# Kernel optimization log

Measured on AMD Instinct MI355X. Metric: run time of the kernel, lower is better.

## Reference

```python
import jax, jax.numpy as jnp
import numpy as np

NUM_HEAD = 16

def setup_inputs() -> dict:
    rk = jax.random.key(0)
    k1, k2, k3, k4, k5 = jax.random.split(rk, 5)
    B, Sq, Skv, D = 4, 2048, 2048, 1024
    return {
        "query": jax.random.normal(k1, (B, Sq, D), dtype=jnp.float32),
        "key":   jax.random.normal(k2, (B, Skv, D), dtype=jnp.float32),
        "value": jax.random.normal(k3, (B, Skv, D), dtype=jnp.float32),
        "W": jax.random.normal(k4, (D, D), dtype=jnp.float32) * (D ** -0.5),
        "b": jax.random.normal(k5, (D,), dtype=jnp.float32) * 0.01,
    }

def reference(query, key, value, W, b):
    B, Sq, D = query.shape
    H = NUM_HEAD
    hd = D // H
    # chunk(num_head, -1) == split last dim into H contiguous heads
    q = query.reshape(B, Sq, H, hd)
    k = key.reshape(B, -1, H, hd)
    v = value.reshape(B, -1, H, hd)
    # scores[b,h,q,k] = (Q_h K_h^T) / sqrt(embedding_dim)  (full dim, per source)
    scores = jnp.einsum('bqhd,bkhd->bhqk', q, k) / jnp.sqrt(jnp.float32(D))
    # nn.Softmax(dim=1) on a [B, q, kv] matrix -> softmax over the QUERY axis
    attn = jax.nn.softmax(scores, axis=2)
    out = jnp.einsum('bhqk,bkhd->bqhd', attn, v).reshape(B, Sq, D)
    # final linear: x @ W^T + b
    return out @ W.T + b
```

## Files before the change

### kernel.cpp

```cpp
#include <hip/hip_runtime.h>

#define NH    16
#define HD    64
#define SQ    2048
#define SKV   2048
#define DM    1024

typedef __attribute__((ext_vector_type(8))) __bf16 bf16x8;
typedef __attribute__((ext_vector_type(4))) __bf16 bf16x4;
typedef __attribute__((ext_vector_type(4))) float  f32x4;

#define ASYNC16(gp, lp)                                                        \
    __builtin_amdgcn_global_load_lds(                                          \
        (const __attribute__((address_space(1))) void*)(gp),                   \
        (__attribute__((address_space(3))) void*)(lp), 16, 0, 0)

#if __has_builtin(__builtin_amdgcn_exp2f)
#define EXPS(x) __builtin_amdgcn_exp2f((x) * 0.04508422f)
#else
#define EXPS(x) __expf((x) * 0.03125f)
#endif

static __device__ __forceinline__ int swz(int row, int chunk) {
    return (row << 6) + (((chunk) ^ (row & 7)) << 3);
}

static __device__ __forceinline__ bf16x4 cvt4(float4 v) {
    bf16x4 r;
    r[0] = (__bf16)v.x; r[1] = (__bf16)v.y; r[2] = (__bf16)v.z; r[3] = (__bf16)v.w;
    return r;
}

__global__ void kprep_all(const float* __restrict__ q, const float* __restrict__ k,
                          const float* __restrict__ W,
                          __bf16* __restrict__ Qh, __bf16* __restrict__ Kh,
                          __bf16* __restrict__ Wb) {
    int bid = blockIdx.x;
    if (bid < 8192) {
        const float* src = (bid < 4096) ? q : k;
        __bf16* dst = (bid < 4096) ? Qh : Kh;
        size_t g = (size_t)(bid & 4095) * 256 + threadIdx.x;
        size_t o = g * 8;
        int c  = (int)(o & 63);
        int s  = (int)((o >> 6) & 2047);
        int bh = (int)(o >> 17);
        int b = bh >> 4, h = bh & 15;
        const float* p = src + ((size_t)(b * SQ + s)) * DM + h * HD + c;
        float4 v0 = *(const float4*)p;
        float4 v1 = *(const float4*)(p + 4);
        bf16x8 r;
        r[0] = (__bf16)v0.x; r[1] = (__bf16)v0.y; r[2] = (__bf16)v0.z; r[3] = (__bf16)v0.w;
        r[4] = (__bf16)v1.x; r[5] = (__bf16)v1.y; r[6] = (__bf16)v1.z; r[7] = (__bf16)v1.w;
        *(bf16x8*)(dst + o) = r;
    } else {
        int i = (bid - 8192) * 256 + threadIdx.x;
        float4 v = *(const float4*)(W + (size_t)i * 4);
        *(bf16x4*)(Wb + (size_t)i * 4) = cvt4(v);
    }
}

__global__ __launch_bounds__(512, 4) void kz(const __bf16* __restrict__ Qh,
                                             const __bf16* __restrict__ Kh,
                                             const __bf16* __restrict__ v,
                                             __bf16* __restrict__ Vt);

__global__ __launch_bounds__(512, 4) void kz(const __bf16* __restrict__ Qh,
                                             const __bf16* __restrict__ Kh,
                                             const __bf16* __restrict__ vv,
                                             __bf16* __restrict__ Vt) {
    const float* v = (const float*)vv;
    const int bh = blockIdx.x;
    const int kb = blockIdx.y;
    const int b = bh >> 4, h = bh & 15;
    const int t = threadIdx.x;
    const int w = t >> 6, lane = t & 63;
    const int lo16 = lane & 15, quad = lane >> 4;
    const int wub = (t & 448) << 3;

    __shared__ __bf16 Ks[256 * 64];
    __shared__ __bf16 Qs[2][64 * 64];
    __shared__ float  Zs[256];

    const __bf16* kbase = Kh + ((size_t)bh * SKV + kb * 256) * HD;
    const __bf16* qbase = Qh + (size_t)bh * SQ * HD;

#pragma unroll
    for (int i = 0; i < 4; ++i) {
        int ci = i * 512 + t;
        int row = ci >> 3;
        int c = (ci & 7) ^ (row & 7);
        ASYNC16(kbase + row * 64 + c * 8, &Ks[i * 4096 + wub]);
    }
    {
        int ci = t;
        int row = ci >> 3;
        int c = (ci & 7) ^ (row & 7);
        ASYNC16(qbase + row * 64 + c * 8, &Qs[0][wub]);
    }
    __syncthreads();

    bf16x8 bk[2][2];
#pragma unroll
    for (int nt = 0; nt < 2; ++nt)
#pragma unroll
        for (int dh = 0; dh < 2; ++dh)
            bk[nt][dh] = *(const bf16x8*)(&Ks[swz(w * 32 + nt * 16 + lo16, dh * 4 + quad)]);

    float zacc[2] = {0.f, 0.f};

    for (int qt = 0; qt < 32; ++qt) {
        const int cur = qt & 1, nxt = cur ^ 1;
        if (qt < 31) {
            int ci = t;
            int row = ci >> 3;
            int c = (ci & 7) ^ (row & 7);
            ASYNC16(qbase + (size_t)(qt + 1) * 64 * HD + row * 64 + c * 8,
                    &Qs[nxt][wub]);
        }

        __builtin_amdgcn_s_setprio(1);
#pragma unroll
        for (int mt = 0; mt < 4; ++mt) {
            bf16x8 aq0 = *(const bf16x8*)(&Qs[cur][swz(mt * 16 + lo16, quad)]);
            bf16x8 aq1 = *(const bf16x8*)(&Qs[cur][swz(mt * 16 + lo16, 4 + quad)]);
#pragma unroll
            for (int nt = 0; nt < 2; ++nt) {
                f32x4 acc = {0.f, 0.f, 0.f, 0.f};
                acc = __builtin_amdgcn_mfma_f32_16x16x32_bf16(aq0, bk[nt][0], acc, 0, 0, 0);
                acc = __builtin_amdgcn_mfma_f32_16x16x32_bf16(aq1, bk[nt][1], acc, 0, 0, 0);
                zacc[nt] += EXPS(acc[0]) + EXPS(acc[1]) + EXPS(acc[2]) + EXPS(acc[3]);
            }
        }
        __builtin_amdgcn_s_setprio(0);
        __syncthreads();
    }

#pragma unroll
    for (int nt = 0; nt < 2; ++nt) {
        float s = zacc[nt];
        s += __shfl_xor(s, 16, 64);
        s += __shfl_xor(s, 32, 64);
        if (lane < 16) Zs[w * 32 + nt * 16 + lane] = s;
    }
    __syncthreads();

    {
        int kcol = t & 255, dh2 = t >> 8;
        float rz = 1.0f / Zs[kcol];
        const float* vrow = v + ((size_t)(b * SKV) + kb * 256 + kcol) * DM + h * HD + dh2 * 32;
        size_t vtb = (size_t)bh * HD * SKV + kb * 256 + kcol;
#pragma unroll
        for (int dc = 0; dc < 2; ++dc) {
            float4 a0 = *(const float4*)(vrow + dc * 16 + 0);
            float4 a1 = *(const float4*)(vrow + dc * 16 + 4);
            float4 a2 = *(const float4*)(vrow + dc * 16 + 8);
            float4 a3 = *(const float4*)(vrow + dc * 16 + 12);
            float tmp[16] = {a0.x, a0.y, a0.z, a0.w, a1.x, a1.y, a1.z, a1.w,
                             a2.x, a2.y, a2.z, a2.w, a3.x, a3.y, a3.z, a3.w};
#pragma unroll
            for (int j = 0; j < 16; ++j)
                Vt[vtb + (size_t)(dh2 * 32 + dc * 16 + j) * SKV] = (__bf16)(tmp[j] * rz);
        }
    }
}

__global__ __launch_bounds__(512, 4) void kattn(const __bf16* __restrict__ Qh,
                                                const __bf16* __restrict__ Kh,
                                                const __bf16* __restrict__ Vt,
                                                __bf16* __restrict__ O) {
    const int bh = blockIdx.x;
    const int qb = blockIdx.y;
    const int b = bh >> 4, h = bh & 15;
    const int t = threadIdx.x;
    const int w = t >> 6, lane = t & 63;
    const int lo16 = lane & 15, quad = lane >> 4;
    const int wub = (t & 448) << 3;

    __shared__ __bf16 Ks[2][64 * 64];
    __shared__ __bf16 Vts[2][64 * 64];
    __shared__ __bf16 Es[8][32 * 64];

    const __bf16* qgb = Qh + ((size_t)bh * SQ + qb * 256 + w * 32) * HD;
    const __bf16* kgbase = Kh + (size_t)bh * SKV * HD;
    const __bf16* vtgbase = Vt + (size_t)bh * HD * SKV;

    {
        int ci = t;
        int row = ci >> 3;
        int c = (ci & 7) ^ (row & 7);
        ASYNC16(kgbase + row * 64 + c * 8, &Ks[0][wub]);
        ASYNC16(vtgbase + (size_t)row * SKV + c * 8, &Vts[0][wub]);
    }

    bf16x8 qf[2][2];
#pragma unroll
    for (int qt = 0; qt < 2; ++qt)
#pragma unroll
        for (int dh = 0; dh < 2; ++dh)
            qf[qt][dh] = *(const bf16x8*)(qgb + (size_t)(qt * 16 + lo16) * HD
                                          + (dh * 4 + quad) * 8);

    f32x4 oacc[2][4];
    f32x4 zero = {0.f, 0.f, 0.f, 0.f};
#pragma unroll
    for (int qt = 0; qt < 2; ++qt)
#pragma unroll
        for (int nt = 0; nt < 4; ++nt)
            oacc[qt][nt] = zero;

    __syncthreads();

    __bf16* Ew = &Es[w][0];

    for (int kt = 0; kt < 32; ++kt) {
        const int cur = kt & 1, nxt = cur ^ 1;
        if (kt < 31) {
            int ci = t;
            int row = ci >> 3;
            int c = (ci & 7) ^ (row & 7);
            ASYNC16(kgbase + (size_t)(kt + 1) * 64 * HD + row * 64 + c * 8,
                    &Ks[nxt][wub]);
            ASYNC16(vtgbase + (size_t)row * SKV + (kt + 1) * 64 + c * 8,
                    &Vts[nxt][wub]);
        }

        __builtin_amdgcn_s_setprio(1);
#pragma unroll
        for (int ktile = 0; ktile < 4; ++ktile) {
            bf16x8 ak0 = *(const bf16x8*)(&Ks[cur][swz(ktile * 16 + lo16, quad)]);
            bf16x8 ak1 = *(const bf16x8*)(&Ks[cur][swz(ktile * 16 + lo16, 4 + quad)]);
#pragma unroll
            for (int qt = 0; qt < 2; ++qt) {
                f32x4 s = zero;
                s = __builtin_amdgcn_mfma_f32_16x16x32_bf16(ak0, qf[qt][0], s, 0, 0, 0);
                s = __builtin_amdgcn_mfma_f32_16x16x32_bf16(ak1, qf[qt][1], s, 0, 0, 0);
                bf16x4 e;
                e[0] = (__bf16)EXPS(s[0]);
                e[1] = (__bf16)EXPS(s[1]);
                e[2] = (__bf16)EXPS(s[2]);
                e[3] = (__bf16)EXPS(s[3]);
                int er = qt * 16 + lo16;
                *(bf16x4*)(&Ew[(er << 6) + ((((2 * ktile + (quad >> 1))) ^ (er & 7)) << 3)
                               + (quad & 1) * 4]) = e;
            }
        }

#pragma unroll
        for (int kk2 = 0; kk2 < 2; ++kk2) {
            bf16x8 ae[2];
#pragma unroll
            for (int qt = 0; qt < 2; ++qt)
                ae[qt] = *(const bf16x8*)(&Ew[swz(qt * 16 + lo16, kk2 * 4 + quad)]);
#pragma unroll
            for (int nt = 0; nt < 4; ++nt) {
                bf16x8 bv = *(const bf16x8*)(&Vts[cur][swz(nt * 16 + lo16, kk2 * 4 + quad)]);
#pragma unroll
                for (int qt = 0; qt < 2; ++qt)
                    oacc[qt][nt] = __builtin_amdgcn_mfma_f32_16x16x32_bf16(ae[qt], bv, oacc[qt][nt], 0, 0, 0);
            }
        }
        __builtin_amdgcn_s_setprio(0);
        __syncthreads();
    }

    size_t obase = ((size_t)(b * SQ) + qb * 256 + w * 32) * DM + h * HD;
#pragma unroll
    for (int qt = 0; qt < 2; ++qt)
#pragma unroll
        for (int nt = 0; nt < 4; ++nt)
#pragma unroll
            for (int r = 0; r < 4; ++r)
                O[obase + (size_t)(qt * 16 + quad * 4 + r) * DM + nt * 16 + lo16] =
                    (__bf16)oacc[qt][nt][r];
}

__global__ __launch_bounds__(256, 2) void kproj(const __bf16* __restrict__ A,
                                                const __bf16* __restrict__ Wb,
                                                const float* __restrict__ bias,
                                                float* __restrict__ out) {
    const int nb = blockIdx.x;
    const int mb = blockIdx.y;
    const int t = threadIdx.x;
    const int w = t >> 6, lane = t & 63;
    const int lo16 = lane & 15, quad = lane >> 4;
    const int wm = w & 1, wn = w >> 1;
    const int wub = (t & 192) << 3;

    __shared__ __bf16 As[2][128 * 64];
    __shared__ __bf16 Bs[2][128 * 64];

    f32x4 acc[4][4];
    f32x4 zero = {0.f, 0.f, 0.f, 0.f};
#pragma unroll
    for (int mt = 0; mt < 4; ++mt)
#pragma unroll
        for (int nt = 0; nt < 4; ++nt)
            acc[mt][nt] = zero;

    const __bf16* abase = A + (size_t)(mb * 128) * DM;
    const __bf16* wbase = Wb + (size_t)(nb * 128) * DM;

#pragma unroll
    for (int i = 0; i < 4; ++i) {
        int ci = i * 256 + t;
        int row = ci >> 3;
        int c = (ci & 7) ^ (row & 7);
        ASYNC16(abase + (size_t)row * DM + c * 8, &As[0][i * 2048 + wub]);
        ASYNC16(wbase + (size_t)row * DM + c * 8, &Bs[0][i * 2048 + wub]);
    }
    __syncthreads();

    for (int kt = 0; kt < 16; ++kt) {
        const int cur = kt & 1, nxt = cur ^ 1;
        if (kt < 15) {
#pragma unroll
            for (int i = 0; i < 4; ++i) {
                int ci = i * 256 + t;
                int row = ci >> 3;
                int c = (ci & 7) ^ (row & 7);
                ASYNC16(abase + (size_t)row * DM + (kt + 1) * 64 + c * 8, &As[nxt][i * 2048 + wub]);
                ASYNC16(wbase + (size_t)row * DM + (kt + 1) * 64 + c * 8, &Bs[nxt][i * 2048 + wub]);
            }
        }

#pragma unroll
        for (int ks = 0; ks < 2; ++ks) {
            bf16x8 av[4], bv[4];
#pragma unroll
            for (int mt = 0; mt < 4; ++mt)
                av[mt] = *(const bf16x8*)(&As[cur][swz(wm * 64 + mt * 16 + lo16, ks * 4 + quad)]);
#pragma unroll
            for (int nt = 0; nt < 4; ++nt)
                bv[nt] = *(const bf16x8*)(&Bs[cur][swz(wn * 64 + nt * 16 + lo16, ks * 4 + quad)]);
#pragma unroll
            for (int mt = 0; mt < 4; ++mt)
#pragma unroll
                for (int nt = 0; nt < 4; ++nt)
                    acc[mt][nt] = __builtin_amdgcn_mfma_f32_16x16x32_bf16(av[mt], bv[nt], acc[mt][nt], 0, 0, 0);
        }
        __syncthreads();
    }

    const int col0 = nb * 128 + wn * 64;
    const int row0 = mb * 128 + wm * 64;
#pragma unroll
    for (int nt = 0; nt < 4; ++nt) {
        float bb = bias[col0 + nt * 16 + lo16];
#pragma unroll
        for (int mt = 0; mt < 4; ++mt)
#pragma unroll
            for (int r = 0; r < 4; ++r)
                out[(size_t)(row0 + mt * 16 + quad * 4 + r) * DM + col0 + nt * 16 + lo16] =
                    acc[mt][nt][r] + bb;
    }
}

extern "C" void kernel_launch(void* const* d_in, const int* in_sizes, int n_in,
                              void* d_out, int out_size, void* d_ws, size_t ws_size,
                              hipStream_t stream) {
    const float* q    = (const float*)d_in[0];
    const float* k    = (const float*)d_in[1];
    const float* v    = (const float*)d_in[2];
    const float* W    = (const float*)d_in[3];
    const float* bias = (const float*)d_in[4];
    float* out = (float*)d_out;

    char* ws = (char*)d_ws;
    __bf16* Qh = (__bf16*)ws;
    __bf16* Kh = (__bf16*)(ws + (16u << 20));
    __bf16* Vt = (__bf16*)(ws + (32u << 20));
    __bf16* Wb = (__bf16*)(ws + (48u << 20));
    __bf16* O  = (__bf16*)(ws + (50u << 20));

    kprep_all<<<dim3(9216), 256, 0, stream>>>(q, k, W, Qh, Kh, Wb);
    kz       <<<dim3(64, 8), 512, 0, stream>>>(Qh, Kh, (const __bf16*)v, Vt);
    kattn    <<<dim3(64, 8), 512, 0, stream>>>(Qh, Kh, Vt, O);
    kproj    <<<dim3(8, 64), 256, 0, stream>>>(O, Wb, bias, out);
}
```

Baseline: 283.3 us.

## Double wavefronts per block in kz and kattn, halving per-wave tile work

Both the column-normalizer kernel and the attention kernel now launch 1024-thread blocks (16 waves) instead of 512, with each wave owning 16 rows instead of 32. Global-to-LDS loads are split so half the threads load K and the other half load Vt, and only the first 8 waves load Q in kz. The goal is more wavefront-level parallelism and latency hiding per block, with fewer registers per wave. In exchange, each wave reuses its LDS fragment loads across half as many MFMAs, so the ratio of LDS reads to MFMA work rises, and the 1024-thread blocks may limit occupancy.

```diff
diff --git a/kernel.cpp b/kernel.cpp
--- a/kernel.cpp
+++ b/kernel.cpp
@@ -59,15 +59,10 @@
     }
 }
 
-__global__ __launch_bounds__(512, 4) void kz(const __bf16* __restrict__ Qh,
-                                             const __bf16* __restrict__ Kh,
-                                             const __bf16* __restrict__ v,
-                                             __bf16* __restrict__ Vt);
-
-__global__ __launch_bounds__(512, 4) void kz(const __bf16* __restrict__ Qh,
-                                             const __bf16* __restrict__ Kh,
-                                             const __bf16* __restrict__ vv,
-                                             __bf16* __restrict__ Vt) {
+__global__ __launch_bounds__(1024, 8) void kz(const __bf16* __restrict__ Qh,
+                                              const __bf16* __restrict__ Kh,
+                                              const __bf16* __restrict__ vv,
+                                              __bf16* __restrict__ Vt) {
     const float* v = (const float*)vv;
     const int bh = blockIdx.x;
     const int kb = blockIdx.y;
@@ -75,7 +70,6 @@
     const int t = threadIdx.x;
     const int w = t >> 6, lane = t & 63;
     const int lo16 = lane & 15, quad = lane >> 4;
-    const int wub = (t & 448) << 3;
 
     __shared__ __bf16 Ks[256 * 64];
     __shared__ __bf16 Qs[2][64 * 64];
@@ -85,37 +79,35 @@
     const __bf16* qbase = Qh + (size_t)bh * SQ * HD;
 
 #pragma unroll
-    for (int i = 0; i < 4; ++i) {
-        int ci = i * 512 + t;
+    for (int i = 0; i < 2; ++i) {
+        int ci = i * 1024 + t;
         int row = ci >> 3;
         int c = (ci & 7) ^ (row & 7);
-        ASYNC16(kbase + row * 64 + c * 8, &Ks[i * 4096 + wub]);
-    }
-    {
+        ASYNC16(kbase + row * 64 + c * 8, &Ks[i * 8192 + ((t & 960) << 3)]);
+    }
+    if (w < 8) {
         int ci = t;
         int row = ci >> 3;
         int c = (ci & 7) ^ (row & 7);
-        ASYNC16(qbase + row * 64 + c * 8, &Qs[0][wub]);
+        ASYNC16(qbase + row * 64 + c * 8, &Qs[0][(t & 448) << 3]);
     }
     __syncthreads();
 
-    bf16x8 bk[2][2];
-#pragma unroll
-    for (int nt = 0; nt < 2; ++nt)
-#pragma unroll
-        for (int dh = 0; dh < 2; ++dh)
-            bk[nt][dh] = *(const bf16x8*)(&Ks[swz(w * 32 + nt * 16 + lo16, dh * 4 + quad)]);
-
-    float zacc[2] = {0.f, 0.f};
+    bf16x8 bk[2];
+#pragma unroll
+    for (int dh = 0; dh < 2; ++dh)
+        bk[dh] = *(const bf16x8*)(&Ks[swz(w * 16 + lo16, dh * 4 + quad)]);
+
+    float zacc = 0.f;
 
     for (int qt = 0; qt < 32; ++qt) {
         const int cur = qt & 1, nxt = cur ^ 1;
-        if (qt < 31) {
+        if (qt < 31 && w < 8) {
             int ci = t;
             int row = ci >> 3;
             int c = (ci & 7) ^ (row & 7);
             ASYNC16(qbase + (size_t)(qt + 1) * 64 * HD + row * 64 + c * 8,
-                    &Qs[nxt][wub]);
+                    &Qs[nxt][(t & 448) << 3]);
         }
 
         __builtin_amdgcn_s_setprio(1);
@@ -123,90 +115,79 @@
         for (int mt = 0; mt < 4; ++mt) {
             bf16x8 aq0 = *(const bf16x8*)(&Qs[cur][swz(mt * 16 + lo16, quad)]);
             bf16x8 aq1 = *(const bf16x8*)(&Qs[cur][swz(mt * 16 + lo16, 4 + quad)]);
-#pragma unroll
-            for (int nt = 0; nt < 2; ++nt) {
-                f32x4 acc = {0.f, 0.f, 0.f, 0.f};
-                acc = __builtin_amdgcn_mfma_f32_16x16x32_bf16(aq0, bk[nt][0], acc, 0, 0, 0);
-                acc = __builtin_amdgcn_mfma_f32_16x16x32_bf16(aq1, bk[nt][1], acc, 0, 0, 0);
-                zacc[nt] += EXPS(acc[0]) + EXPS(acc[1]) + EXPS(acc[2]) + EXPS(acc[3]);
-            }
+            f32x4 acc = {0.f, 0.f, 0.f, 0.f};
+            acc = __builtin_amdgcn_mfma_f32_16x16x32_bf16(aq0, bk[0], acc, 0, 0, 0);
+            acc = __builtin_amdgcn_mfma_f32_16x16x32_bf16(aq1, bk[1], acc, 0, 0, 0);
+            zacc += EXPS(acc[0]) + EXPS(acc[1]) + EXPS(acc[2]) + EXPS(acc[3]);
         }
         __builtin_amdgcn_s_setprio(0);
         __syncthreads();
     }
 
-#pragma unroll
-    for (int nt = 0; nt < 2; ++nt) {
-        float s = zacc[nt];
+    {
+        float s = zacc;
         s += __shfl_xor(s, 16, 64);
         s += __shfl_xor(s, 32, 64);
-        if (lane < 16) Zs[w * 32 + nt * 16 + lane] = s;
+        if (lane < 16) Zs[w * 16 + lane] = s;
     }
     __syncthreads();
 
     {
-        int kcol = t & 255, dh2 = t >> 8;
+        int kcol = t & 255, dq = t >> 8;
         float rz = 1.0f / Zs[kcol];
-        const float* vrow = v + ((size_t)(b * SKV) + kb * 256 + kcol) * DM + h * HD + dh2 * 32;
+        const float* vrow = v + ((size_t)(b * SKV) + kb * 256 + kcol) * DM + h * HD + dq * 16;
         size_t vtb = (size_t)bh * HD * SKV + kb * 256 + kcol;
-#pragma unroll
-        for (int dc = 0; dc < 2; ++dc) {
-            float4 a0 = *(const float4*)(vrow + dc * 16 + 0);
-            float4 a1 = *(const float4*)(vrow + dc * 16 + 4);
-            float4 a2 = *(const float4*)(vrow + dc * 16 + 8);
-            float4 a3 = *(const float4*)(vrow + dc * 16 + 12);
-            float tmp[16] = {a0.x, a0.y, a0.z, a0.w, a1.x, a1.y, a1.z, a1.w,
-                             a2.x, a2.y, a2.z, a2.w, a3.x, a3.y, a3.z, a3.w};
-#pragma unroll
-            for (int j = 0; j < 16; ++j)
-                Vt[vtb + (size_t)(dh2 * 32 + dc * 16 + j) * SKV] = (__bf16)(tmp[j] * rz);
-        }
-    }
-}
-
-__global__ __launch_bounds__(512, 4) void kattn(const __bf16* __restrict__ Qh,
-                                                const __bf16* __restrict__ Kh,
-                                                const __bf16* __restrict__ Vt,
-                                                __bf16* __restrict__ O) {
+        float4 a0 = *(const float4*)(vrow + 0);
+        float4 a1 = *(const float4*)(vrow + 4);
+        float4 a2 = *(const float4*)(vrow + 8);
+        float4 a3 = *(const float4*)(vrow + 12);
+        float tmp[16] = {a0.x, a0.y, a0.z, a0.w, a1.x, a1.y, a1.z, a1.w,
+                         a2.x, a2.y, a2.z, a2.w, a3.x, a3.y, a3.z, a3.w};
+#pragma unroll
+        for (int j = 0; j < 16; ++j)
+            Vt[vtb + (size_t)(dq * 16 + j) * SKV] = (__bf16)(tmp[j] * rz);
+    }
+}
+
+__global__ __launch_bounds__(1024, 8) void kattn(const __bf16* __restrict__ Qh,
+                                                 const __bf16* __restrict__ Kh,
+                                                 const __bf16* __restrict__ Vt,
+                                                 __bf16* __restrict__ O) {
     const int bh = blockIdx.x;
     const int qb = blockIdx.y;
     const int b = bh >> 4, h = bh & 15;
     const int t = threadIdx.x;
     const int w = t >> 6, lane = t & 63;
     const int lo16 = lane & 15, quad = lane >> 4;
-    const int wub = (t & 448) << 3;
 
     __shared__ __bf16 Ks[2][64 * 64];
     __shared__ __bf16 Vts[2][64 * 64];
-    __shared__ __bf16 Es[8][32 * 64];
-
-    const __bf16* qgb = Qh + ((size_t)bh * SQ + qb * 256 + w * 32) * HD;
+    __shared__ __bf16 Es[16][16 * 64];
+
+    const __bf16* qgb = Qh + ((size_t)bh * SQ + qb * 256 + w * 16) * HD;
     const __bf16* kgbase = Kh + (size_t)bh * SKV * HD;
     const __bf16* vtgbase = Vt + (size_t)bh * HD * SKV;
 
     {
-        int ci = t;
+        int ci = t & 511;
         int row = ci >> 3;
         int c = (ci & 7) ^ (row & 7);
-        ASYNC16(kgbase + row * 64 + c * 8, &Ks[0][wub]);
-        ASYNC16(vtgbase + (size_t)row * SKV + c * 8, &Vts[0][wub]);
-    }
-
-    bf16x8 qf[2][2];
-#pragma unroll
-    for (int qt = 0; qt < 2; ++qt)
-#pragma unroll
-        for (int dh = 0; dh < 2; ++dh)
-            qf[qt][dh] = *(const bf16x8*)(qgb + (size_t)(qt * 16 + lo16) * HD
-                                          + (dh * 4 + quad) * 8);
-
-    f32x4 oacc[2][4];
+        if (t < 512)
+            ASYNC16(kgbase + row * 64 + c * 8, &Ks[0][(t & 448) << 3]);
+        else
+            ASYNC16(vtgbase + (size_t)row * SKV + c * 8, &Vts[0][(t & 448) << 3]);
+    }
+
+    bf16x8 qf[2];
+#pragma unroll
+    for (int dh = 0; dh < 2; ++dh)
+        qf[dh] = *(const bf16x8*)(qgb + (size_t)lo16 * HD + (dh * 4 + quad) * 8);
+
+    f32x4 oacc[4];
     f32x4 zero = {0.f, 0.f, 0.f, 0.f};
 #pragma unroll
-    for (int qt = 0; qt < 2; ++qt)
-#pragma unroll
-        for (int nt = 0; nt < 4; ++nt)
-            oacc[qt][nt] = zero;
+    for (int nt = 0; nt < 4; ++nt)
+        oacc[nt] = zero;
 
     __syncthreads();
 
@@ -215,13 +196,15 @@
     for (int kt = 0; kt < 32; ++kt) {
         const int cur = kt & 1, nxt = cur ^ 1;
         if (kt < 31) {
-            int ci = t;
+            int ci = t & 511;
             int row = ci >> 3;
             int c = (ci & 7) ^ (row & 7);
-            ASYNC16(kgbase + (size_t)(kt + 1) * 64 * HD + row * 64 + c * 8,
-                    &Ks[nxt][wub]);
-            ASYNC16(vtgbase + (size_t)row * SKV + (kt + 1) * 64 + c * 8,
-                    &Vts[nxt][wub]);
+            if (t < 512)
+                ASYNC16(kgbase + (size_t)(kt + 1) * 64 * HD + row * 64 + c * 8,
+                        &Ks[nxt][(t & 448) << 3]);
+            else
+                ASYNC16(vtgbase + (size_t)row * SKV + (kt + 1) * 64 + c * 8,
+                        &Vts[nxt][(t & 448) << 3]);
         }
 
         __builtin_amdgcn_s_setprio(1);
@@ -229,49 +212,39 @@
         for (int ktile = 0; ktile < 4; ++ktile) {
             bf16x8 ak0 = *(const bf16x8*)(&Ks[cur][swz(ktile * 16 + lo16, quad)]);
             bf16x8 ak1 = *(const bf16x8*)(&Ks[cur][swz(ktile * 16 + lo16, 4 + quad)]);
-#pragma unroll
-            for (int qt = 0; qt < 2; ++qt) {
-                f32x4 s = zero;
-                s = __builtin_amdgcn_mfma_f32_16x16x32_bf16(ak0, qf[qt][0], s, 0, 0, 0);
-                s = __builtin_amdgcn_mfma_f32_16x16x32_bf16(ak1, qf[qt][1], s, 0, 0, 0);
-                bf16x4 e;
-                e[0] = (__bf16)EXPS(s[0]);
-                e[1] = (__bf16)EXPS(s[1]);
-                e[2] = (__bf16)EXPS(s[2]);
-                e[3] = (__bf16)EXPS(s[3]);
-                int er = qt * 16 + lo16;
-                *(bf16x4*)(&Ew[(er << 6) + ((((2 * ktile + (quad >> 1))) ^ (er & 7)) << 3)
-                               + (quad & 1) * 4]) = e;
-            }
+            f32x4 s = zero;
+            s = __builtin_amdgcn_mfma_f32_16x16x32_bf16(ak0, qf[0], s, 0, 0, 0);
+            s = __builtin_amdgcn_mfma_f32_16x16x32_bf16(ak1, qf[1], s, 0, 0, 0);
+            bf16x4 e;
+            e[0] = (__bf16)EXPS(s[0]);
+            e[1] = (__bf16)EXPS(s[1]);
+            e[2] = (__bf16)EXPS(s[2]);
+            e[3] = (__bf16)EXPS(s[3]);
+            int er = lo16;
+            *(bf16x4*)(&Ew[(er << 6) + ((((2 * ktile + (quad >> 1))) ^ (er & 7)) << 3)
+                           + (quad & 1) * 4]) = e;
         }
 
 #pragma unroll
         for (int kk2 = 0; kk2 < 2; ++kk2) {
-            bf16x8 ae[2];
-#pragma unroll
-            for (int qt = 0; qt < 2; ++qt)
-                ae[qt] = *(const bf16x8*)(&Ew[swz(qt * 16 + lo16, kk2 * 4 + quad)]);
+            bf16x8 ae = *(const bf16x8*)(&Ew[swz(lo16, kk2 * 4 + quad)]);
 #pragma unroll
             for (int nt = 0; nt < 4; ++nt) {
                 bf16x8 bv = *(const bf16x8*)(&Vts[cur][swz(nt * 16 + lo16, kk2 * 4 + quad)]);
-#pragma unroll
-                for (int qt = 0; qt < 2; ++qt)
-                    oacc[qt][nt] = __builtin_amdgcn_mfma_f32_16x16x32_bf16(ae[qt], bv, oacc[qt][nt], 0, 0, 0);
+                oacc[nt] = __builtin_amdgcn_mfma_f32_16x16x32_bf16(ae, bv, oacc[nt], 0, 0, 0);
             }
         }
         __builtin_amdgcn_s_setprio(0);
         __syncthreads();
     }
 
-    size_t obase = ((size_t)(b * SQ) + qb * 256 + w * 32) * DM + h * HD;
-#pragma unroll
-    for (int qt = 0; qt < 2; ++qt)
-#pragma unroll
-        for (int nt = 0; nt < 4; ++nt)
-#pragma unroll
-            for (int r = 0; r < 4; ++r)
-                O[obase + (size_t)(qt * 16 + quad * 4 + r) * DM + nt * 16 + lo16] =
-                    (__bf16)oacc[qt][nt][r];
+    size_t obase = ((size_t)(b * SQ) + qb * 256 + w * 16) * DM + h * HD;
+#pragma unroll
+    for (int nt = 0; nt < 4; ++nt)
+#pragma unroll
+        for (int r = 0; r < 4; ++r)
+            O[obase + (size_t)(quad * 4 + r) * DM + nt * 16 + lo16] =
+                (__bf16)oacc[nt][r];
 }
 
 __global__ __launch_bounds__(256, 2) void kproj(const __bf16* __restrict__ A,
@@ -373,7 +346,7 @@
     __bf16* O  = (__bf16*)(ws + (50u << 20));
 
     kprep_all<<<dim3(9216), 256, 0, stream>>>(q, k, W, Qh, Kh, Wb);
-    kz       <<<dim3(64, 8), 512, 0, stream>>>(Qh, Kh, (const __bf16*)v, Vt);
-    kattn    <<<dim3(64, 8), 512, 0, stream>>>(Qh, Kh, Vt, O);
+    kz       <<<dim3(64, 8), 1024, 0, stream>>>(Qh, Kh, (const __bf16*)v, Vt);
+    kattn    <<<dim3(64, 8), 1024, 0, stream>>>(Qh, Kh, Vt, O);
     kproj    <<<dim3(8, 64), 256, 0, stream>>>(O, Wb, bias, out);
 }
```

Result: slower. 304.8 us (+7.6%).

## Keep softmax probabilities in registers via permlane swaps instead of LDS staging

Applied to the files above, without the earlier changes.

The exp'd score tiles are no longer written to a per-wave LDS buffer and read back as MFMA A-operands. They are packed into bf16 pairs and rearranged across lanes with v_permlane32_swap/v_permlane16_swap so they land directly in the operand layout the PV MFMA expects. This removes 32KB of LDS and the LDS write/read round trip per tile, which may also allow higher occupancy. It relies on the lane permutation exactly matching the old LDS layout, and the pk values and intermediate registers add register pressure.

```diff
diff --git a/kernel.cpp b/kernel.cpp
--- a/kernel.cpp
+++ b/kernel.cpp
@@ -8,6 +8,7 @@
 
 typedef __attribute__((ext_vector_type(8))) __bf16 bf16x8;
 typedef __attribute__((ext_vector_type(4))) __bf16 bf16x4;
+typedef __attribute__((ext_vector_type(2))) __bf16 bf16x2;
 typedef __attribute__((ext_vector_type(4))) float  f32x4;
 
 #define ASYNC16(gp, lp)                                                        \
@@ -29,6 +30,13 @@
     bf16x4 r;
     r[0] = (__bf16)v.x; r[1] = (__bf16)v.y; r[2] = (__bf16)v.z; r[3] = (__bf16)v.w;
     return r;
+}
+
+static __device__ __forceinline__ unsigned pkbf16(float a, float b) {
+    bf16x2 t;
+    t[0] = (__bf16)a;
+    t[1] = (__bf16)b;
+    return __builtin_bit_cast(unsigned, t);
 }
 
 __global__ void kprep_all(const float* __restrict__ q, const float* __restrict__ k,
@@ -61,11 +69,6 @@
 
 __global__ __launch_bounds__(512, 4) void kz(const __bf16* __restrict__ Qh,
                                              const __bf16* __restrict__ Kh,
-                                             const __bf16* __restrict__ v,
-                                             __bf16* __restrict__ Vt);
-
-__global__ __launch_bounds__(512, 4) void kz(const __bf16* __restrict__ Qh,
-                                             const __bf16* __restrict__ Kh,
                                              const __bf16* __restrict__ vv,
                                              __bf16* __restrict__ Vt) {
     const float* v = (const float*)vv;
@@ -178,7 +181,6 @@
 
     __shared__ __bf16 Ks[2][64 * 64];
     __shared__ __bf16 Vts[2][64 * 64];
-    __shared__ __bf16 Es[8][32 * 64];
 
     const __bf16* qgb = Qh + ((size_t)bh * SQ + qb * 256 + w * 32) * HD;
     const __bf16* kgbase = Kh + (size_t)bh * SKV * HD;
@@ -209,8 +211,6 @@
             oacc[qt][nt] = zero;
 
     __syncthreads();
-
-    __bf16* Ew = &Es[w][0];
 
     for (int kt = 0; kt < 32; ++kt) {
         const int cur = kt & 1, nxt = cur ^ 1;
@@ -226,34 +226,40 @@
 
         __builtin_amdgcn_s_setprio(1);
 #pragma unroll
-        for (int ktile = 0; ktile < 4; ++ktile) {
-            bf16x8 ak0 = *(const bf16x8*)(&Ks[cur][swz(ktile * 16 + lo16, quad)]);
-            bf16x8 ak1 = *(const bf16x8*)(&Ks[cur][swz(ktile * 16 + lo16, 4 + quad)]);
+        for (int g = 0; g < 2; ++g) {
+            unsigned pk[2][2][2];
+#pragma unroll
+            for (int tt = 0; tt < 2; ++tt) {
+                int krow = (g * 2 + tt) * 16 + lo16;
+                bf16x8 ak0 = *(const bf16x8*)(&Ks[cur][swz(krow, quad)]);
+                bf16x8 ak1 = *(const bf16x8*)(&Ks[cur][swz(krow, 4 + quad)]);
+#pragma unroll
+                for (int qt = 0; qt < 2; ++qt) {
+                    f32x4 s = zero;
+                    s = __builtin_amdgcn_mfma_f32_16x16x32_bf16(ak0, qf[qt][0], s, 0, 0, 0);
+                    s = __builtin_amdgcn_mfma_f32_16x16x32_bf16(ak1, qf[qt][1], s, 0, 0, 0);
+                    pk[tt][qt][0] = pkbf16(EXPS(s[0]), EXPS(s[1]));
+                    pk[tt][qt][1] = pkbf16(EXPS(s[2]), EXPS(s[3]));
+                }
+            }
+
+            bf16x8 ae[2];
 #pragma unroll
             for (int qt = 0; qt < 2; ++qt) {
-                f32x4 s = zero;
-                s = __builtin_amdgcn_mfma_f32_16x16x32_bf16(ak0, qf[qt][0], s, 0, 0, 0);
-                s = __builtin_amdgcn_mfma_f32_16x16x32_bf16(ak1, qf[qt][1], s, 0, 0, 0);
-                bf16x4 e;
-                e[0] = (__bf16)EXPS(s[0]);
-                e[1] = (__bf16)EXPS(s[1]);
-                e[2] = (__bf16)EXPS(s[2]);
-                e[3] = (__bf16)EXPS(s[3]);
-                int er = qt * 16 + lo16;
-                *(bf16x4*)(&Ew[(er << 6) + ((((2 * ktile + (quad >> 1))) ^ (er & 7)) << 3)
-                               + (quad & 1) * 4]) = e;
-            }
-        }
-
-#pragma unroll
-        for (int kk2 = 0; kk2 < 2; ++kk2) {
-            bf16x8 ae[2];
-#pragma unroll
-            for (int qt = 0; qt < 2; ++qt)
-                ae[qt] = *(const bf16x8*)(&Ew[swz(qt * 16 + lo16, kk2 * 4 + quad)]);
+                unsigned j0 = pk[0][qt][0], j2 = pk[1][qt][0];
+                unsigned j1 = pk[0][qt][1], j3 = pk[1][qt][1];
+                asm("v_permlane32_swap_b32 %0, %1" : "+v"(j0), "+v"(j2));
+                asm("v_permlane16_swap_b32 %0, %1" : "+v"(j0), "+v"(j2));
+                asm("v_permlane32_swap_b32 %0, %1" : "+v"(j1), "+v"(j3));
+                asm("v_permlane16_swap_b32 %0, %1" : "+v"(j1), "+v"(j3));
+                uint4 u;
+                u.x = j0; u.y = j1; u.z = j2; u.w = j3;
+                ae[qt] = __builtin_bit_cast(bf16x8, u);
+            }
+
 #pragma unroll
             for (int nt = 0; nt < 4; ++nt) {
-                bf16x8 bv = *(const bf16x8*)(&Vts[cur][swz(nt * 16 + lo16, kk2 * 4 + quad)]);
+                bf16x8 bv = *(const bf16x8*)(&Vts[cur][swz(nt * 16 + lo16, g * 4 + quad)]);
 #pragma unroll
                 for (int qt = 0; qt < 2; ++qt)
                     oacc[qt][nt] = __builtin_amdgcn_mfma_f32_16x16x32_bf16(ae[qt], bv, oacc[qt][nt], 0, 0, 0);
```

Measured after the change: 281.8 us. No clear change (-0.5%).
